# Kernel optimization log

Measured on AMD Instinct MI355X. Metric: run time of the kernel, lower is better.

## Reference

```python
import jax, jax.numpy as jnp
import numpy as np

BETA = 1.0
LENGTH = 64                      # lattice side
LATTICE_SIZE = LENGTH * LENGTH   # 4096
SAMPLE_SIZE = 16384
TWO_PI = 2.0 * np.pi


def _make_shift(length: int) -> np.ndarray:
    """Nearest-neighbour shift indices (2, L*L): roll by one site in each
    positive direction on a periodic 2D lattice, matching geometry.get_shift()."""
    idx = np.arange(length * length).reshape(length, length)
    up = np.roll(idx, -1, axis=0).reshape(-1)
    right = np.roll(idx, -1, axis=1).reshape(-1)
    return np.stack([up, right], axis=0).astype(np.int64)


def setup_inputs() -> dict:
    key = jax.random.key(0)
    k_state, = jax.random.split(key, 1)
    state = jax.random.uniform(k_state, (SAMPLE_SIZE, LATTICE_SIZE),
                               dtype=jnp.float32, minval=0.0, maxval=TWO_PI)
    shift = jnp.asarray(_make_shift(LENGTH))  # (2, lattice_size) int64 indices
    return {"state": state, "shift": shift}


def reference(state, shift):
    # state: (S, N) polar angles; shift: (n_shifts, N) neighbour indices.
    # neighbours: (S, n_shifts, N) gather along lattice dim
    neighbours = state[:, shift]
    # hamiltonian = -beta * sum cos(theta_neigh - theta); forward returns -H
    log_density = BETA * jnp.sum(
        jnp.cos(neighbours - state[:, None, :]), axis=(1, 2)
    )[:, None]  # (S, 1), matches keepdim=True
    return log_density
```

## Files before the change

kernel.cpp:

```cpp
#include <hip/hip_runtime.h>


#define LAT_L     64
#define NSITE     4096
#define BLOCK     256
#define PER_THR   (NSITE / BLOCK)
#define NSAMPLE   16384

__global__ __launch_bounds__(BLOCK)
void xy_logdensity_kernel(const float* __restrict__ state, float* __restrict__ out) {
    __shared__ float th[NSITE];
    __shared__ float red[BLOCK / 64];

    const int b = blockIdx.x;
    const int t = threadIdx.x;
    const float* __restrict__ row = state + (size_t)b * NSITE;

    const float4* __restrict__ row4 = (const float4*)row;
    float4* th4 = (float4*)th;
#pragma unroll
    for (int k = 0; k < NSITE / 4 / BLOCK; ++k) {
        th4[t + BLOCK * k] = row4[t + BLOCK * k];
    }
    __syncthreads();

    const float inv2pi = 0.15915494309189535f;
    float sum = 0.0f;
#pragma unroll
    for (int k = 0; k < PER_THR; ++k) {
        const int s = t + BLOCK * k;
        const float ts = th[s];
        const int up    = (s + LAT_L) & (NSITE - 1);
        const int right = (s & ~(LAT_L - 1)) | ((s + 1) & (LAT_L - 1));
        sum += __cosf(th[up] - ts);
        sum += __cosf(th[right] - ts);
        (void)inv2pi;
    }

#pragma unroll
    for (int off = 32; off > 0; off >>= 1)
        sum += __shfl_down(sum, off, 64);
    const int wave = t >> 6;
    if ((t & 63) == 0) red[wave] = sum;
    __syncthreads();
    if (t == 0) {
        out[b] = red[0] + red[1] + red[2] + red[3];
    }
}

extern "C" void kernel_launch(void* const* d_in, const int* in_sizes, int n_in,
                              void* d_out, int out_size, void* d_ws, size_t ws_size,
                              hipStream_t stream) {
    const float* state = (const float*)d_in[0];
    float* out = (float*)d_out;

    xy_logdensity_kernel<<<NSAMPLE, BLOCK, 0, stream>>>(state, out);
}
```

Measured before the change: 348.9 us.

## Double-buffer rows via async global-to-LDS loads with multiple samples per block

Each block now handles 8 samples instead of one. The next row is loaded straight from global memory into a second LDS buffer with global_load_lds while the current row is being reduced, so loads overlap with the cosine work. The right-neighbour index math is replaced by a per-thread precomputed delta, and the output write for each sample is deferred until the next barrier. This trades fewer, longer-lived blocks and twice the LDS per block for overlapped memory traffic. It also depends on the compiler placing the correct waits before the barriers for the asynchronous LDS writes.

After: 358.5 us. 2.8% more time.

```diff
diff --git a/kernel.cpp b/kernel.cpp
--- a/kernel.cpp
+++ b/kernel.cpp
@@ -1,50 +1,78 @@
 #include <hip/hip_runtime.h>
 
 
-#define LAT_L     64
-#define NSITE     4096
-#define BLOCK     256
-#define PER_THR   (NSITE / BLOCK)
-#define NSAMPLE   16384
+#define LAT_L    64
+#define NSITE    4096
+#define BLOCK    256
+#define NSAMPLE  16384
+#define SPB      8
+#define NBLK     (NSAMPLE / SPB)
+
+typedef float f4 __attribute__((ext_vector_type(4)));
+
+__device__ __forceinline__ void prefetch_row(const float* __restrict__ grow,
+                                             float* lbuf, int t) {
+    const int w = t >> 6;
+    const int l = t & 63;
+    const f4* __restrict__ g4 = (const f4*)grow;
+    f4* l4 = (f4*)lbuf;
+#pragma unroll
+    for (int k = 0; k < 4; ++k) {
+        const int base = w * 64 + 256 * k;
+        const __attribute__((address_space(1))) void* gp =
+            (const __attribute__((address_space(1))) void*)(g4 + base + l);
+        __attribute__((address_space(3))) void* lp =
+            (__attribute__((address_space(3))) void*)(l4 + base);
+        __builtin_amdgcn_global_load_lds(gp, lp, 16, 0, 0);
+    }
+}
+
+__device__ __forceinline__ float compute_row(const float* __restrict__ th,
+                                             int t, int rdelta) {
+    float s0 = 0.0f, s1 = 0.0f;
+#pragma unroll
+    for (int k = 0; k < NSITE / BLOCK; ++k) {
+        const int s = t + BLOCK * k;
+        const float ts = th[s];
+        const float tu = th[(s + LAT_L) & (NSITE - 1)];
+        const float tr = th[s + rdelta];
+        s0 += __cosf(tu - ts);
+        s1 += __cosf(tr - ts);
+    }
+    return s0 + s1;
+}
 
 __global__ __launch_bounds__(BLOCK)
 void xy_logdensity_kernel(const float* __restrict__ state, float* __restrict__ out) {
-    __shared__ float th[NSITE];
-    __shared__ float red[BLOCK / 64];
+    __shared__ float buf[2][NSITE];
+    __shared__ float red[2][BLOCK / 64];
 
-    const int b = blockIdx.x;
     const int t = threadIdx.x;
-    const float* __restrict__ row = state + (size_t)b * NSITE;
+    const long base_sample = (long)blockIdx.x * SPB;
+    const int rdelta = ((t & 63) == (LAT_L - 1)) ? -(LAT_L - 1) : 1;
 
-    const float4* __restrict__ row4 = (const float4*)row;
-    float4* th4 = (float4*)th;
+    prefetch_row(state + base_sample * NSITE, buf[0], t);
+
+    for (int i = 0; i < SPB; ++i) {
+        __syncthreads();
+        if (i > 0 && t == 0) {
+            const float* r = red[(i - 1) & 1];
+            out[base_sample + i - 1] = r[0] + r[1] + r[2] + r[3];
+        }
+        if (i + 1 < SPB)
+            prefetch_row(state + (base_sample + i + 1) * NSITE, buf[(i + 1) & 1], t);
+
+        float sum = compute_row(buf[i & 1], t, rdelta);
+
 #pragma unroll
-    for (int k = 0; k < NSITE / 4 / BLOCK; ++k) {
-        th4[t + BLOCK * k] = row4[t + BLOCK * k];
+        for (int off = 32; off > 0; off >>= 1)
+            sum += __shfl_down(sum, off, 64);
+        if ((t & 63) == 0) red[i & 1][t >> 6] = sum;
     }
     __syncthreads();
-
-    const float inv2pi = 0.15915494309189535f;
-    float sum = 0.0f;
-#pragma unroll
-    for (int k = 0; k < PER_THR; ++k) {
-        const int s = t + BLOCK * k;
-        const float ts = th[s];
-        const int up    = (s + LAT_L) & (NSITE - 1);
-        const int right = (s & ~(LAT_L - 1)) | ((s + 1) & (LAT_L - 1));
-        sum += __cosf(th[up] - ts);
-        sum += __cosf(th[right] - ts);
-        (void)inv2pi;
-    }
-
-#pragma unroll
-    for (int off = 32; off > 0; off >>= 1)
-        sum += __shfl_down(sum, off, 64);
-    const int wave = t >> 6;
-    if ((t & 63) == 0) red[wave] = sum;
-    __syncthreads();
     if (t == 0) {
-        out[b] = red[0] + red[1] + red[2] + red[3];
+        const float* r = red[(SPB - 1) & 1];
+        out[base_sample + SPB - 1] = r[0] + r[1] + r[2] + r[3];
     }
 }
 
@@ -54,5 +82,5 @@
     const float* state = (const float*)d_in[0];
     float* out = (float*)d_out;
 
-    xy_logdensity_kernel<<<NSAMPLE, BLOCK, 0, stream>>>(state, out);
+    xy_logdensity_kernel<<<NBLK, BLOCK, 0, stream>>>(state, out);
 }
```

## Assign 16 lanes per sample and stream rows through registers with shuffles

Applied to the files above, without the earlier changes.

Replaces the one-block-per-sample shared-memory approach with a mapping where each 16-lane group processes one sample, walking its 64 rows in registers with a one-row prefetch. Horizontal neighbours come from cross-lane shuffles and vertical neighbours from the previous row held in registers. This removes LDS staging, block barriers and the cross-wave reduction. The cost is less parallelism per sample and a serial load chain per lane, which could limit memory-level parallelism.

Measured after the change: 359.0 us. 2.9% more time.

```diff
diff --git a/kernel.cpp b/kernel.cpp
--- a/kernel.cpp
+++ b/kernel.cpp
@@ -1,51 +1,60 @@
 #include <hip/hip_runtime.h>
 
 
-#define LAT_L     64
-#define NSITE     4096
-#define BLOCK     256
-#define PER_THR   (NSITE / BLOCK)
-#define NSAMPLE   16384
+#define LAT_L    64
+#define NSITE    4096
+#define BLOCK    256
+#define NSAMPLE  16384
+#define SPB      16
+#define NBLK     (NSAMPLE / SPB)
+
+__device__ __forceinline__ float vert_sum(const float4 a, const float4 b) {
+    return __cosf(b.x - a.x) + __cosf(b.y - a.y) +
+           __cosf(b.z - a.z) + __cosf(b.w - a.w);
+}
+
+__device__ __forceinline__ float horiz_sum(const float4 v, const int nbr) {
+    const float n0 = __shfl(v.x, nbr, 64);
+    return __cosf(v.y - v.x) + __cosf(v.z - v.y) +
+           __cosf(v.w - v.z) + __cosf(n0 - v.w);
+}
 
 __global__ __launch_bounds__(BLOCK)
 void xy_logdensity_kernel(const float* __restrict__ state, float* __restrict__ out) {
-    __shared__ float th[NSITE];
-    __shared__ float red[BLOCK / 64];
+    const int t = threadIdx.x;
+    const int l = t & 63;
+    const int w = t >> 6;
+    const int g = l >> 4;
+    const int q = l & 15;
 
-    const int b = blockIdx.x;
-    const int t = threadIdx.x;
-    const float* __restrict__ row = state + (size_t)b * NSITE;
+    const long sample = (long)blockIdx.x * SPB + w * 4 + g;
+    const float4* __restrict__ row = (const float4*)(state + sample * NSITE) + q;
+    const int nbr = (l & 48) | ((l + 1) & 15);
 
-    const float4* __restrict__ row4 = (const float4*)row;
-    float4* th4 = (float4*)th;
-#pragma unroll
-    for (int k = 0; k < NSITE / 4 / BLOCK; ++k) {
-        th4[t + BLOCK * k] = row4[t + BLOCK * k];
+    float4 first = row[0];
+    float4 cur   = first;
+    float4 nxt   = row[16];
+
+    float sum = horiz_sum(cur, nbr);
+
+#pragma unroll 4
+    for (int y = 1; y < LAT_L - 1; ++y) {
+        const float4 pf = row[(y + 1) * 16];
+        sum += vert_sum(cur, nxt);
+        sum += horiz_sum(nxt, nbr);
+        cur = nxt;
+        nxt = pf;
     }
-    __syncthreads();
-
-    const float inv2pi = 0.15915494309189535f;
-    float sum = 0.0f;
-#pragma unroll
-    for (int k = 0; k < PER_THR; ++k) {
-        const int s = t + BLOCK * k;
-        const float ts = th[s];
-        const int up    = (s + LAT_L) & (NSITE - 1);
-        const int right = (s & ~(LAT_L - 1)) | ((s + 1) & (LAT_L - 1));
-        sum += __cosf(th[up] - ts);
-        sum += __cosf(th[right] - ts);
-        (void)inv2pi;
-    }
+    sum += vert_sum(cur, nxt);
+    sum += horiz_sum(nxt, nbr);
+    sum += vert_sum(nxt, first);
 
 #pragma unroll
-    for (int off = 32; off > 0; off >>= 1)
-        sum += __shfl_down(sum, off, 64);
-    const int wave = t >> 6;
-    if ((t & 63) == 0) red[wave] = sum;
-    __syncthreads();
-    if (t == 0) {
-        out[b] = red[0] + red[1] + red[2] + red[3];
-    }
+    for (int off = 8; off > 0; off >>= 1)
+        sum += __shfl_xor(sum, off, 16);
+
+    if (q == 0)
+        out[sample] = sum;
 }
 
 extern "C" void kernel_launch(void* const* d_in, const int* in_sizes, int n_in,
@@ -54,5 +63,5 @@
     const float* state = (const float*)d_in[0];
     float* out = (float*)d_out;
 
-    xy_logdensity_kernel<<<NSAMPLE, BLOCK, 0, stream>>>(state, out);
+    xy_logdensity_kernel<<<NBLK, BLOCK, 0, stream>>>(state, out);
 }
```
